# Optimization experiments

Measured on AMD Instinct MI355X. Metric: run time of the kernel, lower is better.

Reference implementation:

```python
import jax, jax.numpy as jnp
import numpy as np

DIM = 256
HEADS = 8
HEAD_DIM = DIM // HEADS
B = 8
HH, WW = 32, 32
N = HH * WW
TABLE = (2 * HH - 1) * (2 * WW - 1)  # 3969
CPB_HID = 512


def _l2norm(t, eps=1e-12):
    # matches torch F.normalize(dim=-1): x / max(||x||, eps)
    n = jnp.sqrt(jnp.sum(t * t, axis=-1, keepdims=True))
    return t / jnp.maximum(n, eps)


def setup_inputs() -> dict:
    key = jax.random.key(0)
    ks = jax.random.split(key, 12)
    x = jax.random.normal(ks[0], (B, N, DIM), dtype=jnp.float32)
    relative_pos_index = jax.random.randint(ks[1], (N, N), 0, TABLE)
    relative_coords_table = jax.random.normal(ks[2], (TABLE, 2), dtype=jnp.float32)
    s = 0.02
    qkv_w = jax.random.normal(ks[3], (3 * DIM, DIM), dtype=jnp.float32) * s
    qkv_b = jnp.zeros((3 * DIM,), dtype=jnp.float32)
    query_embedding = jax.random.normal(ks[4], (HEADS, 1, HEAD_DIM), dtype=jnp.float32) * s
    # temperature init: log(exp(1/0.24) - 1) so softplus(temperature) = 1/0.24
    temperature = jnp.full((HEADS, 1, 1), float(np.log(np.expm1(1.0 / 0.24))), dtype=jnp.float32)
    proj_w = jax.random.normal(ks[5], (DIM, DIM), dtype=jnp.float32) * s
    proj_b = jnp.zeros((DIM,), dtype=jnp.float32)
    cpb_fc1_w = jax.random.normal(ks[6], (CPB_HID, 2), dtype=jnp.float32) * s
    cpb_fc1_b = jnp.zeros((CPB_HID,), dtype=jnp.float32)
    cpb_fc2_w = jax.random.normal(ks[7], (HEADS, CPB_HID), dtype=jnp.float32) * s
    cpb_fc2_b = jnp.zeros((HEADS,), dtype=jnp.float32)
    return dict(x=x, H=HH, W=WW, relative_pos_index=relative_pos_index,
                relative_coords_table=relative_coords_table,
                qkv_w=qkv_w, qkv_b=qkv_b, query_embedding=query_embedding,
                temperature=temperature, proj_w=proj_w, proj_b=proj_b,
                cpb_fc1_w=cpb_fc1_w, cpb_fc1_b=cpb_fc1_b,
                cpb_fc2_w=cpb_fc2_w, cpb_fc2_b=cpb_fc2_b)


def reference(x, H, W, relative_pos_index, relative_coords_table,
              qkv_w, qkv_b, query_embedding, temperature,
              proj_w, proj_b, cpb_fc1_w, cpb_fc1_b, cpb_fc2_w, cpb_fc2_b):
    Bc, Nc, C = x.shape
    seq_length_scale = jnp.asarray(np.log(HH * WW), dtype=x.dtype)  # from init input_resolution
    # qkv projection -> [B, heads, N, head_dim] each
    qkv = (x @ qkv_w.T + qkv_b).reshape(Bc, Nc, 3 * HEADS, HEAD_DIM).transpose(0, 2, 1, 3)
    q, k, v = qkv[:, :HEADS], qkv[:, HEADS:2 * HEADS], qkv[:, 2 * HEADS:]
    # CPB relative position bias: small MLP over coord table, then NxN gather
    h = jax.nn.relu(relative_coords_table @ cpb_fc1_w.T + cpb_fc1_b)  # [T, 512]
    table = (h @ cpb_fc2_w.T + cpb_fc2_b).T                           # [heads, T]
    rel_bias = table[:, relative_pos_index.reshape(-1)].reshape(HEADS, Nc, Nc)
    # cosine attention with learned temperature
    qn = _l2norm(q) + query_embedding[None]                           # [B, heads, N, hd]
    scale = jax.nn.softplus(temperature) * seq_length_scale           # [heads, 1, 1]
    attn = jnp.einsum('bhnd,bhmd->bhnm', qn * scale[None], _l2norm(k)) + rel_bias[None]
    attn = jax.nn.softmax(attn, axis=-1)
    out = jnp.einsum('bhnm,bhmd->bhnd', attn, v).transpose(0, 2, 1, 3).reshape(Bc, Nc, C)
    return out @ proj_w.T + proj_b
```

## Files before the change

kernel.cpp:

```cpp
#include <hip/hip_runtime.h>
#include <hip/hip_bf16.h>
#include <cstddef>
#include <cstdint>

typedef float v4f __attribute__((ext_vector_type(4)));
typedef short v8s __attribute__((ext_vector_type(8)));
typedef _Float16 v8h __attribute__((ext_vector_type(8)));

__device__ __forceinline__ uint32_t fbits(float x){ uint32_t u; __builtin_memcpy(&u,&x,4); return u; }
__device__ __forceinline__ float ffrom(uint32_t u){ float f; __builtin_memcpy(&f,&u,4); return f; }
__device__ __forceinline__ short bf_rh(float x){ return (short)((fbits(x)+0x8000u)>>16); }
__device__ __forceinline__ uint32_t pack_bf_rh(float a, float b){
    uint32_t ua = fbits(a)+0x8000u, ub = fbits(b)+0x8000u;
#if __has_builtin(__builtin_amdgcn_perm)
    return __builtin_amdgcn_perm(ub, ua, 0x07060302u);
#else
    return (ua>>16) | (ub & 0xFFFF0000u);
#endif
}
__device__ __forceinline__ short f2h(float x){ _Float16 h = (_Float16)x; short s; __builtin_memcpy(&s,&h,2); return s; }
#if __has_builtin(__builtin_amdgcn_exp2f)
#define EXP2(x) __builtin_amdgcn_exp2f(x)
#else
#define EXP2(x) exp2f(x)
#endif

__device__ __forceinline__ void gld16(const void* g, void* l) {
    __builtin_amdgcn_global_load_lds(
        (const __attribute__((address_space(1))) unsigned int*)g,
        (__attribute__((address_space(3))) unsigned int*)l, 16, 0, 0);
}
#define MFMA(a,b,c)  __builtin_amdgcn_mfma_f32_16x16x32_bf16((a),(b),(c),0,0,0)
#define MFMAH(a,b,c) __builtin_amdgcn_mfma_f32_16x16x32_f16((a),(b),(c),0,0,0)

#define LOG2E 1.4426950408889634f

__global__ __launch_bounds__(256)
void fused_qkv(const float* __restrict__ x,   const float* __restrict__ wq,
               const float* __restrict__ wp,  const float* __restrict__ rct,
               const float* __restrict__ fc1w, const float* __restrict__ fc1b,
               const float* __restrict__ fc2w, const float* __restrict__ fc2b,
               const float* __restrict__ qkvb, const float* __restrict__ qe,
               const float* __restrict__ temp, const int* __restrict__ rpi,
               short* __restrict__ qh, short* __restrict__ kh,
               short* __restrict__ vt, unsigned short* __restrict__ tbl_bf,
               short* __restrict__ wph, unsigned long long* __restrict__ bi)
{
    __shared__ __align__(16) char smem[49152];
    int bid  = blockIdx.x;
    int tid  = threadIdx.x;
    int w    = tid >> 6;
    int lane = tid & 63;
    int t    = lane & 15;
    int quad = lane >> 4;
    int lr8  = lane >> 3, lc8 = lane & 7;

    if (bid < 63) {
        float* s1 = (float*)smem;
        float* sb = s1 + 1024;
        float* s2 = sb + 512;
        for (int i = tid; i < 1024; i += 256) s1[i] = fc1w[i];
        for (int i = tid; i < 512;  i += 256) sb[i] = fc1b[i];
        for (int i = tid; i < 4096; i += 256) s2[i] = fc2w[i];
        __syncthreads();
        int rl = tid >> 2, jp = tid & 3;
        bool ok = rl < 63;
        int r = bid * 63 + rl;
        float c0 = ok ? rct[2*r]   : 0.f;
        float c1 = ok ? rct[2*r+1] : 0.f;
        float a[8] = {0,0,0,0,0,0,0,0};
        int j0 = jp * 128;
        #pragma unroll 4
        for (int j = j0; j < j0 + 128; ++j) {
            float hv = fmaxf(c0*s1[2*j] + c1*s1[2*j+1] + sb[j], 0.0f);
            #pragma unroll
            for (int hh = 0; hh < 8; ++hh) a[hh] += hv * s2[hh*512 + j];
        }
        #pragma unroll
        for (int hh = 0; hh < 8; ++hh) {
            a[hh] += __shfl_xor(a[hh], 1);
            a[hh] += __shfl_xor(a[hh], 2);
        }
        if (ok && jp == 0) {
            #pragma unroll
            for (int hh = 0; hh < 8; ++hh)
                tbl_bf[hh*4096 + r] =
                    (unsigned short)bf_rh((a[hh] + fc2b[hh]) * LOG2E);
        }
    } else if (bid < 95) {
        int base8 = (bid - 63) * 256;
        int e0 = (base8 + tid) * 8;
        int m  = e0 >> 8;
        int k  = e0 & 255;
        int kt = k >> 6, c = (k >> 3) & 7;
        float4 f0 = *(const float4*)(wp + e0);
        float4 f1 = *(const float4*)(wp + e0 + 4);
        float v[8] = {f0.x,f0.y,f0.z,f0.w,f1.x,f1.y,f1.z,f1.w};
        v8s hi;
        #pragma unroll
        for (int j = 0; j < 8; ++j) hi[j] = f2h(v[j]);
        int dst = m*256 + kt*64 + ((c ^ (m & 7)) << 3);
        *(v8s*)&wph[dst] = hi;
    } else if (bid < 159) {
        int q16 = bid - 95;
        int grp = tid >> 6;
        #pragma unroll 1
        for (int c = 0; c < 16; ++c) {
            int combo = grp*16 + c;
            int kt = combo >> 2, g = combo & 3;
            unsigned long long pk = 0;
            #pragma unroll
            for (int r = 0; r < 4; ++r) {
                int idx = rpi[(size_t)(q16*16 + quad*4 + r)*1024 + kt*64 + 4*t + g];
                pk |= (unsigned long long)(idx & 0xFFFF) << (16*r);
            }
            bi[((size_t)(q16*16 + kt)*4 + g)*64 + lane] = pk;
        }
    } else {
        short* A0 = (short*)smem;
        short* A1 = A0 + 128*64;
        short* W0 = A1 + 128*64;
        short* W1 = W0 + 64*64;
        int g2 = bid - 159;
        int n0 = (g2 % 12) * 64, m0 = (g2 / 12) * 128;
        int Mw = (w >> 1) * 64, Nw = (w & 1) * 32;

        v4f acc[4][2];
        #pragma unroll
        for (int mt = 0; mt < 4; ++mt)
            #pragma unroll
            for (int nt = 0; nt < 2; ++nt) acc[mt][nt] = (v4f){0,0,0,0};

        #pragma unroll 1
        for (int kt2 = 0; kt2 < 2; ++kt2) {
            __syncthreads();
            #pragma unroll
            for (int half = 0; half < 2; ++half) {
                int kt = kt2*2 + half;
                short* Ad = half ? A1 : A0;
                short* Wd = half ? W1 : W0;
                #pragma unroll
                for (int i = 0; i < 4; ++i) {
                    int rr = w*32 + i*8 + lr8;
                    const float* s = x + (size_t)(m0 + rr)*256 + kt*64 + lc8*8;
                    float4 f0 = *(const float4*)s;
                    float4 f1 = *(const float4*)(s + 4);
                    v8h hv;
                    hv[0]=(_Float16)f0.x; hv[1]=(_Float16)f0.y;
                    hv[2]=(_Float16)f0.z; hv[3]=(_Float16)f0.w;
                    hv[4]=(_Float16)f1.x; hv[5]=(_Float16)f1.y;
                    hv[6]=(_Float16)f1.z; hv[7]=(_Float16)f1.w;
                    *(v8h*)&Ad[rr*64 + ((lc8 ^ lr8) << 3)] = hv;
                }
                #pragma unroll
                for (int i = 0; i < 2; ++i) {
                    int rr = w*16 + i*8 + lr8;
                    const float* s = wq + (size_t)(n0 + rr)*256 + kt*64 + lc8*8;
                    float4 f0 = *(const float4*)s;
                    float4 f1 = *(const float4*)(s + 4);
                    v8h hv;
                    hv[0]=(_Float16)f0.x; hv[1]=(_Float16)f0.y;
                    hv[2]=(_Float16)f0.z; hv[3]=(_Float16)f0.w;
                    hv[4]=(_Float16)f1.x; hv[5]=(_Float16)f1.y;
                    hv[6]=(_Float16)f1.z; hv[7]=(_Float16)f1.w;
                    *(v8h*)&Wd[rr*64 + ((lc8 ^ lr8) << 3)] = hv;
                }
            }
            __syncthreads();
            #pragma unroll
            for (int half = 0; half < 2; ++half) {
                const short* As = half ? A1 : A0;
                const short* Ws = half ? W1 : W0;
                #pragma unroll
                for (int kk = 0; kk < 2; ++kk) {
                    int cp = ((kk*4 + quad) ^ (t & 7)) << 3;
                    v8h bh8[2];
                    #pragma unroll
                    for (int nt = 0; nt < 2; ++nt)
                        bh8[nt] = *(const v8h*)&Ws[(Nw + nt*16 + t)*64 + cp];
                    #pragma unroll
                    for (int mt = 0; mt < 4; ++mt) {
                        v8h ah = *(const v8h*)&As[(Mw + mt*16 + t)*64 + cp];
                        #pragma unroll
                        for (int nt = 0; nt < 2; ++nt)
                            acc[mt][nt] = MFMAH(ah, bh8[nt], acc[mt][nt]);
                    }
                }
            }
        }

        #pragma unroll
        for (int nt = 0; nt < 2; ++nt) {
            float bv = qkvb[n0 + Nw + nt*16 + t];
            #pragma unroll
            for (int mt = 0; mt < 4; ++mt)
                #pragma unroll
                for (int r = 0; r < 4; ++r) acc[mt][nt][r] += bv;
        }

        int which = n0 >> 8;
        if (which < 2) {
            int head = ((n0 + Nw) >> 5) & 7;
            float scale = 0.f;
            if (which == 0)
                scale = log1pf(__expf(temp[head])) * 10.0f;
            #pragma unroll
            for (int mt = 0; mt < 4; ++mt)
                #pragma unroll
                for (int r = 0; r < 4; ++r) {
                    float a0 = acc[mt][0][r], a1 = acc[mt][1][r];
                    float s = a0*a0 + a1*a1;
                    s += __shfl_xor(s, 1); s += __shfl_xor(s, 2);
                    s += __shfl_xor(s, 4); s += __shfl_xor(s, 8);
                    float inv = 1.0f / fmaxf(sqrtf(s), 1e-12f);
                    int m = m0 + Mw + mt*16 + quad*4 + r;
                    int b = m >> 10, nrow = m & 1023;
                    if (which == 0) {
                        size_t rowoff = (((size_t)b*8 + head)*1024 + nrow) * 32;
                        #pragma unroll
                        for (int nt = 0; nt < 2; ++nt) {
                            int d = nt*16 + t;
                            float val = (acc[mt][nt][r] * inv + qe[head*32 + d]) * scale;
                            qh[rowoff + d] = f2h(val);
                        }
                    } else {
                        int kk = nrow & 63;
                        int pp = (kk & 3)*16 + (kk >> 2);
                        int prow = (nrow & ~63) | pp;
                        int swk = (kk >> 3) & 3;
                        size_t rowoff = (((size_t)b*8 + head)*1024 + prow) * 32;
                        #pragma unroll
                        for (int nt = 0; nt < 2; ++nt) {
                            int d = nt*16 + t;
                            int dpos = (((d >> 3) ^ swk) << 3) | (d & 7);
                            kh[rowoff + dpos] = f2h(acc[mt][nt][r] * inv);
                        }
                    }
                }
        } else {
            __syncthreads();
            short* VT = (short*)smem;
            #pragma unroll
            for (int mt = 0; mt < 4; ++mt)
                #pragma unroll
                for (int nt = 0; nt < 2; ++nt) {
                    int cl = Nw + nt*16 + t;
                    #pragma unroll
                    for (int r = 0; r < 4; ++r) {
                        int rl = Mw + mt*16 + quad*4 + r;
                        VT[cl*136 + rl] = bf_rh(acc[mt][nt][r]);
                    }
                }
            __syncthreads();
            int b = m0 >> 10;
            int keybase = m0 & 1023;
            int headbase = ((n0 - 512) >> 5) & 7;
            int cl = tid >> 2;
            int dim = cl & 31;
            int hd  = headbase + (cl >> 5);
            size_t obase = (((size_t)b*8 + hd)*32 + dim) * 1024 + keybase;
            #pragma unroll
            for (int pz = 0; pz < 4; ++pz) {
                int ci  = (tid & 3) * 4 + pz;
                int ktl = ci >> 3, c = ci & 7;
                v8s val = *(const v8s*)&VT[cl*136 + ktl*64 + c*8];
                *(v8s*)&vt[obase + ktl*64 + ((c ^ (dim & 7)) << 3)] = val;
            }
        }
    }
}

__global__ __launch_bounds__(256)
void attn_mfma(const short* __restrict__ qh, const short* __restrict__ kh,
               const short* __restrict__ vt,
               const unsigned long long* __restrict__ bi,
               const unsigned short* __restrict__ tbl_bf,
               short* __restrict__ yh)
{
    __shared__ __align__(16) short Kh[2][2048];
    __shared__ __align__(16) short Vts[2][2048];
    __shared__ __align__(16) short Psb[4*16*68];
    __shared__ __align__(16) unsigned short tb16[4096];

    int bh  = blockIdx.x & 63;
    int qt2 = blockIdx.x >> 6;
    int h   = bh & 7;
    int b   = bh >> 3;
    int tid = threadIdx.x;
    int w    = tid >> 6;
    int lane = tid & 63;
    int t    = lane & 15;
    int quad = lane >> 4;
    int lr8 = lane >> 3, lc8 = lane & 7;

    {
        const v8s* src = (const v8s*)(tbl_bf + h*4096);
        v8s* dst = (v8s*)tb16;
        dst[tid]       = src[tid];
        dst[tid + 256] = src[tid + 256];
    }

    size_t qoff = ((size_t)bh*1024 + qt2*64 + w*16 + t) * 32 + quad*8;
    v8h qf = *(const v8h*)(qh + qoff);

    v4f Oacc[2] = {{0,0,0,0},{0,0,0,0}};
    float lsum[4] = {0,0,0,0};

    size_t kgbase = (size_t)bh * 32768;
    const unsigned long long* bmb = bi + (size_t)(qt2*4 + w)*4096 + lane;
    int qrow0 = qt2*64 + w*16 + quad*4;
    int swzS = (quad ^ ((t >> 1) & 3)) << 3;

    if (w < 2) {
        gld16(kh + kgbase + (w*2+0)*512 + lane*8, &Kh[0][(w*2+0)*512]);
        gld16(kh + kgbase + (w*2+1)*512 + lane*8, &Kh[0][(w*2+1)*512]);
    } else {
        int v0 = w - 2;
        gld16(vt + kgbase + (size_t)(v0*16 + lr8)*1024 + lc8*8,     &Vts[0][(v0*2+0)*512]);
        gld16(vt + kgbase + (size_t)(v0*16 + 8 + lr8)*1024 + lc8*8, &Vts[0][(v0*2+1)*512]);
    }
    unsigned long long curb[4];
    #pragma unroll
    for (int g = 0; g < 4; ++g) curb[g] = bmb[g*64];

    #pragma unroll 1
    for (int kt = 0; kt < 16; ++kt) {
        int cur = kt & 1;
        __syncthreads();
        unsigned long long nxtb[4];
        if (kt < 15) {
            int nkt = kt + 1, nb = cur ^ 1;
            if (w < 2) {
                gld16(kh + kgbase + (size_t)nkt*2048 + (w*2+0)*512 + lane*8,
                      &Kh[nb][(w*2+0)*512]);
                gld16(kh + kgbase + (size_t)nkt*2048 + (w*2+1)*512 + lane*8,
                      &Kh[nb][(w*2+1)*512]);
            } else {
                int v0 = w - 2;
                gld16(vt + kgbase + (size_t)(v0*16 + lr8)*1024 + nkt*64 + lc8*8,
                      &Vts[nb][(v0*2+0)*512]);
                gld16(vt + kgbase + (size_t)(v0*16 + 8 + lr8)*1024 + nkt*64 + lc8*8,
                      &Vts[nb][(v0*2+1)*512]);
            }
            #pragma unroll
            for (int g = 0; g < 4; ++g) nxtb[g] = bmb[nkt*256 + g*64];
        }

        v4f S[4];
        #pragma unroll
        for (int g = 0; g < 4; ++g) {
            unsigned long long cb = curb[g];
            v4f c;
            c[0] = ffrom((uint32_t)tb16[(uint32_t)cb & 0xFFFFu] << 16);
            c[1] = ffrom((uint32_t)tb16[(uint32_t)(cb >> 16) & 0xFFFFu] << 16);
            c[2] = ffrom((uint32_t)tb16[(uint32_t)(cb >> 32) & 0xFFFFu] << 16);
            c[3] = ffrom((uint32_t)tb16[(uint32_t)(cb >> 48)] << 16);
            v8h kb = *(const v8h*)&Kh[cur][(g*16 + t)*32 + swzS];
            S[g] = MFMAH(qf, kb, c);
        }

        #pragma unroll
        for (int r = 0; r < 4; ++r) {
            float p0 = EXP2(S[0][r]);
            float p1 = EXP2(S[1][r]);
            float p2 = EXP2(S[2][r]);
            float p3 = EXP2(S[3][r]);
            lsum[r] += (p0 + p1) + (p2 + p3);
            uint2 pk;
            pk.x = pack_bf_rh(p0, p1);
            pk.y = pack_bf_rh(p2, p3);
            *(uint2*)&Psb[(w*16 + quad*4 + r)*68 + t*4] = pk;
        }

        #pragma unroll
        for (int ks = 0; ks < 2; ++ks) {
            v8s pf = *(const v8s*)&Psb[(w*16 + t)*68 + ks*32 + quad*8];
            int vsw = ((ks*4 + quad) ^ (t & 7)) << 3;
            #pragma unroll
            for (int g = 0; g < 2; ++g) {
                v8s vf = *(const v8s*)&Vts[cur][(g*16 + t)*64 + vsw];
                Oacc[g] = MFMA(pf, vf, Oacc[g]);
            }
        }
        #pragma unroll
        for (int g = 0; g < 4; ++g) curb[g] = nxtb[g];
    }

    #pragma unroll
    for (int r = 0; r < 4; ++r) {
        float l = lsum[r];
        l += __shfl_xor(l, 1); l += __shfl_xor(l, 2);
        l += __shfl_xor(l, 4); l += __shfl_xor(l, 8);
        float inv = 1.0f / l;
        int qrow = qrow0 + r;
        int m = b*1024 + qrow;
        size_t mbase = (size_t)m * 256;
        int mk = m & 7;
        #pragma unroll
        for (int g = 0; g < 2; ++g) {
            float o = Oacc[g][r] * inv;
            int c = h*4 + g*2 + (t >> 3);
            int chp = ((c ^ mk) << 3) | (t & 7);
            yh[mbase + chp] = f2h(o);
        }
    }
}

__global__ __launch_bounds__(256)
void gemm_proj(const short* __restrict__ Ah_g, const short* __restrict__ Wh_g,
               const float* __restrict__ bias, float* __restrict__ C, int N)
{
    __shared__ __align__(16) short As[2][4096];
    __shared__ __align__(16) short Ws[2][4096];

    int tid  = threadIdx.x;
    int w    = tid >> 6;
    int lane = tid & 63;
    int t    = lane & 15;
    int quad = lane >> 4;
    int m0 = blockIdx.y * 64, n0 = blockIdx.x * 64;
    int Mw = (w >> 1) * 32, Nw = (w & 1) * 32;

    v4f acc[2][2];
    #pragma unroll
    for (int mt = 0; mt < 2; ++mt)
        #pragma unroll
        for (int nt = 0; nt < 2; ++nt) acc[mt][nt] = (v4f){0,0,0,0};

    int lr8 = lane >> 3, lc8 = lane & 7;
    #pragma unroll 1
    for (int kt2 = 0; kt2 < 2; ++kt2) {
        __syncthreads();
        #pragma unroll
        for (int half = 0; half < 2; ++half) {
            int kt = kt2*2 + half;
            #pragma unroll
            for (int i = 0; i < 2; ++i) {
                size_t grow = (size_t)(m0 + w*16 + i*8 + lr8) * 256 + kt*64 + lc8*8;
                gld16(Ah_g + grow, &As[half][(w*16 + i*8) * 64]);
            }
            #pragma unroll
            for (int i = 0; i < 2; ++i) {
                size_t grow = (size_t)(n0 + w*16 + i*8 + lr8) * 256 + kt*64 + lc8*8;
                gld16(Wh_g + grow, &Ws[half][(w*16 + i*8) * 64]);
            }
        }
        __syncthreads();
        #pragma unroll
        for (int half = 0; half < 2; ++half) {
            #pragma unroll
            for (int kk = 0; kk < 2; ++kk) {
                int cp = ((kk*4 + quad) ^ (t & 7)) << 3;
                v8h bh8[2];
                #pragma unroll
                for (int nt = 0; nt < 2; ++nt)
                    bh8[nt] = *(const v8h*)&Ws[half][(Nw + nt*16 + t)*64 + cp];
                #pragma unroll
                for (int mt = 0; mt < 2; ++mt) {
                    v8h ah = *(const v8h*)&As[half][(Mw + mt*16 + t)*64 + cp];
                    #pragma unroll
                    for (int nt = 0; nt < 2; ++nt)
                        acc[mt][nt] = MFMAH(ah, bh8[nt], acc[mt][nt]);
                }
            }
        }
    }

    #pragma unroll
    for (int nt = 0; nt < 2; ++nt) {
        float bv = bias[n0 + Nw + nt*16 + t];
        #pragma unroll
        for (int mt = 0; mt < 2; ++mt)
            #pragma unroll
            for (int r = 0; r < 4; ++r) acc[mt][nt][r] += bv;
    }
    #pragma unroll
    for (int mt = 0; mt < 2; ++mt)
        #pragma unroll
        for (int r = 0; r < 4; ++r) {
            int m = m0 + Mw + mt*16 + quad*4 + r;
            #pragma unroll
            for (int nt = 0; nt < 2; ++nt)
                C[(size_t)m * N + n0 + Nw + nt*16 + t] = acc[mt][nt][r];
        }
}

extern "C" void kernel_launch(void* const* d_in, const int* in_sizes, int n_in,
                              void* d_out, int out_size, void* d_ws, size_t ws_size,
                              hipStream_t stream)
{
    const float* x     = (const float*)d_in[0];
    const int*   rpi   = (const int*)d_in[3];
    const float* rct   = (const float*)d_in[4];
    const float* qkvw  = (const float*)d_in[5];
    const float* qkvb  = (const float*)d_in[6];
    const float* qe    = (const float*)d_in[7];
    const float* temp  = (const float*)d_in[8];
    const float* projw = (const float*)d_in[9];
    const float* projb = (const float*)d_in[10];
    const float* fc1w  = (const float*)d_in[11];
    const float* fc1b  = (const float*)d_in[12];
    const float* fc2w  = (const float*)d_in[13];
    const float* fc2b  = (const float*)d_in[14];

    char* p = (char*)d_ws;
    unsigned short* tbl_bf = (unsigned short*)p; p += 65536;
    short* y     = (short*)p;  p += 4194304;
    short* wph   = (short*)p;  p += 131072;
    short* qh    = (short*)p;  p += 4194304;
    short* kh    = (short*)p;  p += 4194304;
    short* vt    = (short*)p;  p += 4194304;
    unsigned long long* bi = (unsigned long long*)p; p += 2097152;
    float* out   = (float*)d_out;

    fused_qkv<<<927, 256, 0, stream>>>(x, qkvw, projw, rct,
                                       fc1w, fc1b, fc2w, fc2b,
                                       qkvb, qe, temp, rpi,
                                       qh, kh, vt, tbl_bf, wph, bi);

    attn_mfma<<<1024, 256, 0, stream>>>(qh, kh, vt, bi, tbl_bf, y);

    dim3 g2(256/64, 8192/64);
    gemm_proj<<<g2, 256, 0, stream>>>(y, wph, projb, out, 256);
}
```

Before: 150.6 us.

## Keep full-K x tile resident in LDS and loop over three N tiles per block

The QKV GEMM blocks now load a 128-row x tile covering the full K=256 into LDS once and reuse it across three 64-column weight tiles, instead of reloading and reconverting x for each of 12 column tiles. The grid shrinks from 927 to 415 blocks, and the side tasks (CPB table, proj weight conversion, bias index packing) move to the back of the grid. This cuts redundant global reads and fp16 conversion of x. In exchange LDS grows to about 113KB per block, which limits occupancy to one block per CU, and each block does serialized work with added barriers. The smaller grid gives less parallelism across the many CUs.

```diff
diff --git a/kernel.cpp b/kernel.cpp
--- a/kernel.cpp
+++ b/kernel.cpp
@@ -46,7 +46,7 @@
                short* __restrict__ vt, unsigned short* __restrict__ tbl_bf,
                short* __restrict__ wph, unsigned long long* __restrict__ bi)
 {
-    __shared__ __align__(16) char smem[49152];
+    __shared__ __align__(16) char smem[115712];
     int bid  = blockIdx.x;
     int tid  = threadIdx.x;
     int w    = tid >> 6;
@@ -55,103 +55,36 @@
     int quad = lane >> 4;
     int lr8  = lane >> 3, lc8 = lane & 7;
 
-    if (bid < 63) {
-        float* s1 = (float*)smem;
-        float* sb = s1 + 1024;
-        float* s2 = sb + 512;
-        for (int i = tid; i < 1024; i += 256) s1[i] = fc1w[i];
-        for (int i = tid; i < 512;  i += 256) sb[i] = fc1b[i];
-        for (int i = tid; i < 4096; i += 256) s2[i] = fc2w[i];
-        __syncthreads();
-        int rl = tid >> 2, jp = tid & 3;
-        bool ok = rl < 63;
-        int r = bid * 63 + rl;
-        float c0 = ok ? rct[2*r]   : 0.f;
-        float c1 = ok ? rct[2*r+1] : 0.f;
-        float a[8] = {0,0,0,0,0,0,0,0};
-        int j0 = jp * 128;
-        #pragma unroll 4
-        for (int j = j0; j < j0 + 128; ++j) {
-            float hv = fmaxf(c0*s1[2*j] + c1*s1[2*j+1] + sb[j], 0.0f);
-            #pragma unroll
-            for (int hh = 0; hh < 8; ++hh) a[hh] += hv * s2[hh*512 + j];
-        }
-        #pragma unroll
-        for (int hh = 0; hh < 8; ++hh) {
-            a[hh] += __shfl_xor(a[hh], 1);
-            a[hh] += __shfl_xor(a[hh], 2);
-        }
-        if (ok && jp == 0) {
-            #pragma unroll
-            for (int hh = 0; hh < 8; ++hh)
-                tbl_bf[hh*4096 + r] =
-                    (unsigned short)bf_rh((a[hh] + fc2b[hh]) * LOG2E);
-        }
-    } else if (bid < 95) {
-        int base8 = (bid - 63) * 256;
-        int e0 = (base8 + tid) * 8;
-        int m  = e0 >> 8;
-        int k  = e0 & 255;
-        int kt = k >> 6, c = (k >> 3) & 7;
-        float4 f0 = *(const float4*)(wp + e0);
-        float4 f1 = *(const float4*)(wp + e0 + 4);
-        float v[8] = {f0.x,f0.y,f0.z,f0.w,f1.x,f1.y,f1.z,f1.w};
-        v8s hi;
-        #pragma unroll
-        for (int j = 0; j < 8; ++j) hi[j] = f2h(v[j]);
-        int dst = m*256 + kt*64 + ((c ^ (m & 7)) << 3);
-        *(v8s*)&wph[dst] = hi;
-    } else if (bid < 159) {
-        int q16 = bid - 95;
-        int grp = tid >> 6;
+    if (bid < 256) {
+        short* A  = (short*)smem;
+        short* Ws = (short*)(smem + 65536);
+        short* VT = (short*)(smem + 98304);
+        int m0 = (bid >> 2) * 128;
+        int ng = bid & 3;
+        int Mw = (w >> 1) * 64, Nw = (w & 1) * 32;
+
+        #pragma unroll
+        for (int kt = 0; kt < 4; ++kt)
+            #pragma unroll
+            for (int i = 0; i < 4; ++i) {
+                int rr = w*32 + i*8 + lr8;
+                const float* s = x + (size_t)(m0 + rr)*256 + kt*64 + lc8*8;
+                float4 f0 = *(const float4*)s;
+                float4 f1 = *(const float4*)(s + 4);
+                v8h hv;
+                hv[0]=(_Float16)f0.x; hv[1]=(_Float16)f0.y;
+                hv[2]=(_Float16)f0.z; hv[3]=(_Float16)f0.w;
+                hv[4]=(_Float16)f1.x; hv[5]=(_Float16)f1.y;
+                hv[6]=(_Float16)f1.z; hv[7]=(_Float16)f1.w;
+                *(v8h*)&A[rr*256 + kt*64 + ((lc8 ^ lr8) << 3)] = hv;
+            }
+
         #pragma unroll 1
-        for (int c = 0; c < 16; ++c) {
-            int combo = grp*16 + c;
-            int kt = combo >> 2, g = combo & 3;
-            unsigned long long pk = 0;
-            #pragma unroll
-            for (int r = 0; r < 4; ++r) {
-                int idx = rpi[(size_t)(q16*16 + quad*4 + r)*1024 + kt*64 + 4*t + g];
-                pk |= (unsigned long long)(idx & 0xFFFF) << (16*r);
-            }
-            bi[((size_t)(q16*16 + kt)*4 + g)*64 + lane] = pk;
-        }
-    } else {
-        short* A0 = (short*)smem;
-        short* A1 = A0 + 128*64;
-        short* W0 = A1 + 128*64;
-        short* W1 = W0 + 64*64;
-        int g2 = bid - 159;
-        int n0 = (g2 % 12) * 64, m0 = (g2 / 12) * 128;
-        int Mw = (w >> 1) * 64, Nw = (w & 1) * 32;
-
-        v4f acc[4][2];
-        #pragma unroll
-        for (int mt = 0; mt < 4; ++mt)
-            #pragma unroll
-            for (int nt = 0; nt < 2; ++nt) acc[mt][nt] = (v4f){0,0,0,0};
-
-        #pragma unroll 1
-        for (int kt2 = 0; kt2 < 2; ++kt2) {
-            __syncthreads();
-            #pragma unroll
-            for (int half = 0; half < 2; ++half) {
-                int kt = kt2*2 + half;
-                short* Ad = half ? A1 : A0;
-                short* Wd = half ? W1 : W0;
-                #pragma unroll
-                for (int i = 0; i < 4; ++i) {
-                    int rr = w*32 + i*8 + lr8;
-                    const float* s = x + (size_t)(m0 + rr)*256 + kt*64 + lc8*8;
-                    float4 f0 = *(const float4*)s;
-                    float4 f1 = *(const float4*)(s + 4);
-                    v8h hv;
-                    hv[0]=(_Float16)f0.x; hv[1]=(_Float16)f0.y;
-                    hv[2]=(_Float16)f0.z; hv[3]=(_Float16)f0.w;
-                    hv[4]=(_Float16)f1.x; hv[5]=(_Float16)f1.y;
-                    hv[6]=(_Float16)f1.z; hv[7]=(_Float16)f1.w;
-                    *(v8h*)&Ad[rr*64 + ((lc8 ^ lr8) << 3)] = hv;
-                }
+        for (int ii = 0; ii < 3; ++ii) {
+            int n0 = (ng*3 + ii) * 64;
+
+            #pragma unroll
+            for (int kt = 0; kt < 4; ++kt)
                 #pragma unroll
                 for (int i = 0; i < 2; ++i) {
                     int rr = w*16 + i*8 + lr8;
@@ -163,109 +96,174 @@
                     hv[2]=(_Float16)f0.z; hv[3]=(_Float16)f0.w;
                     hv[4]=(_Float16)f1.x; hv[5]=(_Float16)f1.y;
                     hv[6]=(_Float16)f1.z; hv[7]=(_Float16)f1.w;
-                    *(v8h*)&Wd[rr*64 + ((lc8 ^ lr8) << 3)] = hv;
+                    *(v8h*)&Ws[rr*256 + kt*64 + ((lc8 ^ lr8) << 3)] = hv;
                 }
-            }
             __syncthreads();
-            #pragma unroll
-            for (int half = 0; half < 2; ++half) {
-                const short* As = half ? A1 : A0;
-                const short* Ws = half ? W1 : W0;
+
+            v4f acc[4][2];
+            #pragma unroll
+            for (int mt = 0; mt < 4; ++mt)
+                #pragma unroll
+                for (int nt = 0; nt < 2; ++nt) acc[mt][nt] = (v4f){0,0,0,0};
+
+            #pragma unroll
+            for (int kt = 0; kt < 4; ++kt)
                 #pragma unroll
                 for (int kk = 0; kk < 2; ++kk) {
                     int cp = ((kk*4 + quad) ^ (t & 7)) << 3;
                     v8h bh8[2];
                     #pragma unroll
                     for (int nt = 0; nt < 2; ++nt)
-                        bh8[nt] = *(const v8h*)&Ws[(Nw + nt*16 + t)*64 + cp];
+                        bh8[nt] = *(const v8h*)&Ws[(Nw + nt*16 + t)*256 + kt*64 + cp];
                     #pragma unroll
                     for (int mt = 0; mt < 4; ++mt) {
-                        v8h ah = *(const v8h*)&As[(Mw + mt*16 + t)*64 + cp];
+                        v8h ah = *(const v8h*)&A[(Mw + mt*16 + t)*256 + kt*64 + cp];
                         #pragma unroll
                         for (int nt = 0; nt < 2; ++nt)
                             acc[mt][nt] = MFMAH(ah, bh8[nt], acc[mt][nt]);
                     }
                 }
-            }
-        }
-
-        #pragma unroll
-        for (int nt = 0; nt < 2; ++nt) {
-            float bv = qkvb[n0 + Nw + nt*16 + t];
-            #pragma unroll
-            for (int mt = 0; mt < 4; ++mt)
-                #pragma unroll
-                for (int r = 0; r < 4; ++r) acc[mt][nt][r] += bv;
-        }
-
-        int which = n0 >> 8;
-        if (which < 2) {
-            int head = ((n0 + Nw) >> 5) & 7;
-            float scale = 0.f;
-            if (which == 0)
-                scale = log1pf(__expf(temp[head])) * 10.0f;
-            #pragma unroll
-            for (int mt = 0; mt < 4; ++mt)
-                #pragma unroll
-                for (int r = 0; r < 4; ++r) {
-                    float a0 = acc[mt][0][r], a1 = acc[mt][1][r];
-                    float s = a0*a0 + a1*a1;
-                    s += __shfl_xor(s, 1); s += __shfl_xor(s, 2);
-                    s += __shfl_xor(s, 4); s += __shfl_xor(s, 8);
-                    float inv = 1.0f / fmaxf(sqrtf(s), 1e-12f);
-                    int m = m0 + Mw + mt*16 + quad*4 + r;
-                    int b = m >> 10, nrow = m & 1023;
-                    if (which == 0) {
-                        size_t rowoff = (((size_t)b*8 + head)*1024 + nrow) * 32;
-                        #pragma unroll
-                        for (int nt = 0; nt < 2; ++nt) {
-                            int d = nt*16 + t;
-                            float val = (acc[mt][nt][r] * inv + qe[head*32 + d]) * scale;
-                            qh[rowoff + d] = f2h(val);
-                        }
-                    } else {
-                        int kk = nrow & 63;
-                        int pp = (kk & 3)*16 + (kk >> 2);
-                        int prow = (nrow & ~63) | pp;
-                        int swk = (kk >> 3) & 3;
-                        size_t rowoff = (((size_t)b*8 + head)*1024 + prow) * 32;
-                        #pragma unroll
-                        for (int nt = 0; nt < 2; ++nt) {
-                            int d = nt*16 + t;
-                            int dpos = (((d >> 3) ^ swk) << 3) | (d & 7);
-                            kh[rowoff + dpos] = f2h(acc[mt][nt][r] * inv);
+
+            #pragma unroll
+            for (int nt = 0; nt < 2; ++nt) {
+                float bv = qkvb[n0 + Nw + nt*16 + t];
+                #pragma unroll
+                for (int mt = 0; mt < 4; ++mt)
+                    #pragma unroll
+                    for (int r = 0; r < 4; ++r) acc[mt][nt][r] += bv;
+            }
+
+            int which = n0 >> 8;
+            if (which < 2) {
+                int head = ((n0 + Nw) >> 5) & 7;
+                float scale = 0.f;
+                if (which == 0)
+                    scale = log1pf(__expf(temp[head])) * 10.0f;
+                #pragma unroll
+                for (int mt = 0; mt < 4; ++mt)
+                    #pragma unroll
+                    for (int r = 0; r < 4; ++r) {
+                        float a0 = acc[mt][0][r], a1 = acc[mt][1][r];
+                        float s = a0*a0 + a1*a1;
+                        s += __shfl_xor(s, 1); s += __shfl_xor(s, 2);
+                        s += __shfl_xor(s, 4); s += __shfl_xor(s, 8);
+                        float inv = 1.0f / fmaxf(sqrtf(s), 1e-12f);
+                        int m = m0 + Mw + mt*16 + quad*4 + r;
+                        int b = m >> 10, nrow = m & 1023;
+                        if (which == 0) {
+                            size_t rowoff = (((size_t)b*8 + head)*1024 + nrow) * 32;
+                            #pragma unroll
+                            for (int nt = 0; nt < 2; ++nt) {
+                                int d = nt*16 + t;
+                                float val = (acc[mt][nt][r] * inv + qe[head*32 + d]) * scale;
+                                qh[rowoff + d] = f2h(val);
+                            }
+                        } else {
+                            int kk2 = nrow & 63;
+                            int pp = (kk2 & 3)*16 + (kk2 >> 2);
+                            int prow = (nrow & ~63) | pp;
+                            int swk = (kk2 >> 3) & 3;
+                            size_t rowoff = (((size_t)b*8 + head)*1024 + prow) * 32;
+                            #pragma unroll
+                            for (int nt = 0; nt < 2; ++nt) {
+                                int d = nt*16 + t;
+                                int dpos = (((d >> 3) ^ swk) << 3) | (d & 7);
+                                kh[rowoff + dpos] = f2h(acc[mt][nt][r] * inv);
+                            }
                         }
                     }
+            } else {
+                __syncthreads();
+                #pragma unroll
+                for (int mt = 0; mt < 4; ++mt)
+                    #pragma unroll
+                    for (int nt = 0; nt < 2; ++nt) {
+                        int cl = Nw + nt*16 + t;
+                        #pragma unroll
+                        for (int r = 0; r < 4; ++r) {
+                            int rl = Mw + mt*16 + quad*4 + r;
+                            VT[cl*136 + rl] = bf_rh(acc[mt][nt][r]);
+                        }
+                    }
+                __syncthreads();
+                int b = m0 >> 10;
+                int keybase = m0 & 1023;
+                int headbase = ((n0 - 512) >> 5) & 7;
+                int cl = tid >> 2;
+                int dim = cl & 31;
+                int hd  = headbase + (cl >> 5);
+                size_t obase = (((size_t)b*8 + hd)*32 + dim) * 1024 + keybase;
+                #pragma unroll
+                for (int pz = 0; pz < 4; ++pz) {
+                    int ci  = (tid & 3) * 4 + pz;
+                    int ktl = ci >> 3, c = ci & 7;
+                    v8s val = *(const v8s*)&VT[cl*136 + ktl*64 + c*8];
+                    *(v8s*)&vt[obase + ktl*64 + ((c ^ (dim & 7)) << 3)] = val;
                 }
-        } else {
+            }
             __syncthreads();
-            short* VT = (short*)smem;
-            #pragma unroll
-            for (int mt = 0; mt < 4; ++mt)
-                #pragma unroll
-                for (int nt = 0; nt < 2; ++nt) {
-                    int cl = Nw + nt*16 + t;
-                    #pragma unroll
-                    for (int r = 0; r < 4; ++r) {
-                        int rl = Mw + mt*16 + quad*4 + r;
-                        VT[cl*136 + rl] = bf_rh(acc[mt][nt][r]);
-                    }
-                }
-            __syncthreads();
-            int b = m0 >> 10;
-            int keybase = m0 & 1023;
-            int headbase = ((n0 - 512) >> 5) & 7;
-            int cl = tid >> 2;
-            int dim = cl & 31;
-            int hd  = headbase + (cl >> 5);
-            size_t obase = (((size_t)b*8 + hd)*32 + dim) * 1024 + keybase;
-            #pragma unroll
-            for (int pz = 0; pz < 4; ++pz) {
-                int ci  = (tid & 3) * 4 + pz;
-                int ktl = ci >> 3, c = ci & 7;
-                v8s val = *(const v8s*)&VT[cl*136 + ktl*64 + c*8];
-                *(v8s*)&vt[obase + ktl*64 + ((c ^ (dim & 7)) << 3)] = val;
-            }
+        }
+    } else if (bid < 319) {
+        float* s1 = (float*)smem;
+        float* sb = s1 + 1024;
+        float* s2 = sb + 512;
+        int cbid = bid - 256;
+        for (int i = tid; i < 1024; i += 256) s1[i] = fc1w[i];
+        for (int i = tid; i < 512;  i += 256) sb[i] = fc1b[i];
+        for (int i = tid; i < 4096; i += 256) s2[i] = fc2w[i];
+        __syncthreads();
+        int rl = tid >> 2, jp = tid & 3;
+        bool ok = rl < 63;
+        int r = cbid * 63 + rl;
+        float c0 = ok ? rct[2*r]   : 0.f;
+        float c1 = ok ? rct[2*r+1] : 0.f;
+        float a[8] = {0,0,0,0,0,0,0,0};
+        int j0 = jp * 128;
+        #pragma unroll 4
+        for (int j = j0; j < j0 + 128; ++j) {
+            float hv = fmaxf(c0*s1[2*j] + c1*s1[2*j+1] + sb[j], 0.0f);
+            #pragma unroll
+            for (int hh = 0; hh < 8; ++hh) a[hh] += hv * s2[hh*512 + j];
+        }
+        #pragma unroll
+        for (int hh = 0; hh < 8; ++hh) {
+            a[hh] += __shfl_xor(a[hh], 1);
+            a[hh] += __shfl_xor(a[hh], 2);
+        }
+        if (ok && jp == 0) {
+            #pragma unroll
+            for (int hh = 0; hh < 8; ++hh)
+                tbl_bf[hh*4096 + r] =
+                    (unsigned short)bf_rh((a[hh] + fc2b[hh]) * LOG2E);
+        }
+    } else if (bid < 351) {
+        int base8 = (bid - 319) * 256;
+        int e0 = (base8 + tid) * 8;
+        int m  = e0 >> 8;
+        int k  = e0 & 255;
+        int kt = k >> 6, c = (k >> 3) & 7;
+        float4 f0 = *(const float4*)(wp + e0);
+        float4 f1 = *(const float4*)(wp + e0 + 4);
+        float v[8] = {f0.x,f0.y,f0.z,f0.w,f1.x,f1.y,f1.z,f1.w};
+        v8s hi;
+        #pragma unroll
+        for (int j = 0; j < 8; ++j) hi[j] = f2h(v[j]);
+        int dst = m*256 + kt*64 + ((c ^ (m & 7)) << 3);
+        *(v8s*)&wph[dst] = hi;
+    } else {
+        int q16 = bid - 351;
+        int grp = tid >> 6;
+        #pragma unroll 1
+        for (int c = 0; c < 16; ++c) {
+            int combo = grp*16 + c;
+            int kt = combo >> 2, g = combo & 3;
+            unsigned long long pk = 0;
+            #pragma unroll
+            for (int r = 0; r < 4; ++r) {
+                int idx = rpi[(size_t)(q16*16 + quad*4 + r)*1024 + kt*64 + 4*t + g];
+                pk |= (unsigned long long)(idx & 0xFFFF) << (16*r);
+            }
+            bi[((size_t)(q16*16 + kt)*4 + g)*64 + lane] = pk;
         }
     }
 }
@@ -513,7 +511,7 @@
     unsigned long long* bi = (unsigned long long*)p; p += 2097152;
     float* out   = (float*)d_out;
 
-    fused_qkv<<<927, 256, 0, stream>>>(x, qkvw, projw, rct,
+    fused_qkv<<<415, 256, 0, stream>>>(x, qkvw, projw, rct,
                                        fc1w, fc1b, fc2w, fc2b,
                                        qkvb, qe, temp, rpi,
                                        qh, kh, vt, tbl_bf, wph, bi);
```

After: 165.4 us. 1.1x slower.
